# Kernel tuning notes

Hardware: AMD Instinct MI355X
Metric: run time of the kernel (lower is better)

## Reference

```python
import jax, jax.numpy as jnp
import numpy as np

VIS_DIM = 768
LBL_DIM = 128
HID = 256
VIS_W = 0.4
LBL_W = 0.6
TEMP = 1.0
EPS = 1e-12  # torch F.normalize default eps


def setup_inputs() -> dict:
    key = jax.random.key(0)
    ks = jax.random.split(key, 8)
    B, N = 32, 4096
    visual_feats = jax.random.normal(ks[0], (B, N, VIS_DIM), dtype=jnp.float32)
    label_context = jax.random.normal(ks[1], (B, LBL_DIM), dtype=jnp.float32)
    visual_mask = jnp.ones((B, N), dtype=bool)
    # scorer MLP params (stored [in, out] for x @ W)
    W1 = jax.random.normal(ks[2], (VIS_DIM, HID), dtype=jnp.float32) / np.sqrt(VIS_DIM)
    b1 = jnp.zeros((HID,), dtype=jnp.float32)
    W2 = jax.random.normal(ks[3], (HID, 1), dtype=jnp.float32) / np.sqrt(HID)
    b2 = jnp.zeros((1,), dtype=jnp.float32)
    # label -> visual projection
    Wp = jax.random.normal(ks[4], (LBL_DIM, VIS_DIM), dtype=jnp.float32) / np.sqrt(LBL_DIM)
    bp = jnp.zeros((VIS_DIM,), dtype=jnp.float32)
    return {
        "visual_feats": visual_feats,
        "label_context": label_context,
        "W1": W1, "b1": b1, "W2": W2, "b2": b2, "Wp": Wp, "bp": bp,
        "visual_mask": visual_mask,
        "k": 192,
    }


def _l2norm(x):
    n = jnp.linalg.norm(x, axis=-1, keepdims=True)
    return x / jnp.maximum(n, EPS)


def reference(visual_feats, label_context, W1, b1, W2, b2, Wp, bp, visual_mask, k):
    B, N, D = visual_feats.shape
    # scoring MLP: [B,N,D] -> [B,N]
    h = jnp.maximum(jnp.einsum('bnd,dh->bnh', visual_feats, W1) + b1, 0.0)
    visual_scores = (jnp.einsum('bnh,ho->bno', h, W2) + b2)[..., 0]
    # label projection [B,D] then cosine similarity against each patch
    label_proj = label_context @ Wp + bp              # [B, D]
    vis_n = _l2norm(visual_feats)                     # [B, N, D]
    lbl_n = _l2norm(label_proj)[:, None, :]           # [B, 1, D]
    label_scores = jnp.sum(vis_n * lbl_n, axis=-1)    # [B, N]
    combined = (VIS_W * visual_scores + LBL_W * label_scores) / TEMP
    combined = jnp.where(visual_mask, combined, -jnp.inf)
    k = min(int(k), N)
    topk_scores, topk_indices = jax.lax.top_k(combined, k)   # [B, k]
    selected_feats = jnp.take_along_axis(visual_feats, topk_indices[..., None], axis=1)
    return selected_feats, topk_indices
```

## Files before the change

kernel.cpp:

```cpp
#include <hip/hip_runtime.h>
#include <hip/hip_bf16.h>

#define B_   32
#define N_   4096
#define D_   768
#define HID_ 256

#define SX 64.0f
#define SW 1024.0f
#define INV_S (1.0f / 65536.0f)

typedef unsigned long long ull;
typedef _Float16 half8 __attribute__((ext_vector_type(8)));
typedef float f32x16 __attribute__((ext_vector_type(16)));

__global__ __launch_bounds__(256) void wsplit_kernel(
    const float* __restrict__ W1, _Float16* __restrict__ whi,
    _Float16* __restrict__ wlo) {
  int c = blockIdx.x;
  int h = threadIdx.x;
  half8 vh, vl;
#pragma unroll
  for (int j = 0; j < 8; ++j) {
    float w = W1[(size_t)(c * 8 + j) * 256 + h] * SW;
    _Float16 hi = (_Float16)w;
    vh[j] = hi;
    vl[j] = (_Float16)(w - (float)hi);
  }
  *(half8*)&whi[((size_t)c * 256 + h) * 8] = vh;
  *(half8*)&wlo[((size_t)c * 256 + h) * 8] = vl;
}

__global__ __launch_bounds__(256) void proj_norm_kernel(
    const float* __restrict__ lc, const float* __restrict__ Wp,
    const float* __restrict__ bp, float* __restrict__ lbl_n) {
  int b = blockIdx.x;
  int t = threadIdx.x;
  __shared__ float s_lc[128];
  __shared__ float s_out[768];
  __shared__ float s_red[4];

  if (t < 128) s_lc[t] = lc[b * 128 + t];
  __syncthreads();

  float sumsq = 0.f;
  for (int d = t; d < D_; d += 256) {
    float acc = bp[d];
    for (int k = 0; k < 128; ++k) acc += s_lc[k] * Wp[k * D_ + d];
    s_out[d] = acc;
    sumsq += acc * acc;
  }
  for (int off = 32; off >= 1; off >>= 1) sumsq += __shfl_xor(sumsq, off);
  if ((t & 63) == 0) s_red[t >> 6] = sumsq;
  __syncthreads();
  float tot = s_red[0] + s_red[1] + s_red[2] + s_red[3];
  float inv = 1.f / fmaxf(sqrtf(tot), 1e-12f);
  for (int d = t; d < D_; d += 256) lbl_n[b * D_ + d] = s_out[d] * inv;
}

__global__ __launch_bounds__(256, 2) void score2_kernel(
    const float* __restrict__ X, const _Float16* __restrict__ Whi,
    const _Float16* __restrict__ Wlo, const float* __restrict__ b1,
    const float* __restrict__ W2, const float* __restrict__ b2,
    const float* __restrict__ lbl_n, float* __restrict__ scores) {
  __shared__ __align__(16) _Float16 sW[2][2][4][256][8];
  __shared__ float sLbl[768];
  __shared__ float sB1[256];
  __shared__ float sW2[256];

  const int t = threadIdx.x;
  const int w = t >> 6;
  const int l = t & 63;
  const int l5 = l >> 5;
  const int ln = l & 31;
  const int pb = blockIdx.x * 128;
  const int batch = pb >> 12;
  const int patch = pb + w * 32 + ln;
  const float* xrow = X + (size_t)patch * D_;

  for (int i = t; i < D_; i += 256) sLbl[i] = lbl_n[batch * D_ + i];
  sB1[t] = b1[t];
  sW2[t] = W2[t];

  f32x16 acc[8];
#pragma unroll
  for (int mt = 0; mt < 8; ++mt)
#pragma unroll
    for (int r = 0; r < 16; ++r) acc[mt][r] = 0.f;

  const float4* gWh = (const float4*)Whi;
  const float4* gWl = (const float4*)Wlo;

  float4 wh0 = gWh[0 * 256 + t], wh1 = gWh[1 * 256 + t],
         wh2 = gWh[2 * 256 + t], wh3 = gWh[3 * 256 + t];
  float4 wl0 = gWl[0 * 256 + t], wl1 = gWl[1 * 256 + t],
         wl2 = gWl[2 * 256 + t], wl3 = gWl[3 * 256 + t];
  float4 cx0 = *(const float4*)(xrow + l5 * 8);
  float4 cx1 = *(const float4*)(xrow + l5 * 8 + 4);
  float4 cx2 = *(const float4*)(xrow + 16 + l5 * 8);
  float4 cx3 = *(const float4*)(xrow + 16 + l5 * 8 + 4);
  {
    float4* dh = (float4*)&sW[0][0][0][0][0];
    float4* dl = (float4*)&sW[0][1][0][0][0];
    dh[0 * 256 + t] = wh0; dh[1 * 256 + t] = wh1;
    dh[2 * 256 + t] = wh2; dh[3 * 256 + t] = wh3;
    dl[0 * 256 + t] = wl0; dl[1 * 256 + t] = wl1;
    dl[2 * 256 + t] = wl2; dl[3 * 256 + t] = wl3;
  }
  __syncthreads();

  float sq = 0.f, dt = 0.f;

  for (int s = 0; s < 24; ++s) {
    const int cur = s & 1;
    float4 nx0, nx1, nx2, nx3;
    if (s < 23) {
      const int sn = s + 1;
      wh0 = gWh[(size_t)sn * 1024 + 0 * 256 + t];
      wh1 = gWh[(size_t)sn * 1024 + 1 * 256 + t];
      wh2 = gWh[(size_t)sn * 1024 + 2 * 256 + t];
      wh3 = gWh[(size_t)sn * 1024 + 3 * 256 + t];
      wl0 = gWl[(size_t)sn * 1024 + 0 * 256 + t];
      wl1 = gWl[(size_t)sn * 1024 + 1 * 256 + t];
      wl2 = gWl[(size_t)sn * 1024 + 2 * 256 + t];
      wl3 = gWl[(size_t)sn * 1024 + 3 * 256 + t];
      nx0 = *(const float4*)(xrow + sn * 32 + l5 * 8);
      nx1 = *(const float4*)(xrow + sn * 32 + l5 * 8 + 4);
      nx2 = *(const float4*)(xrow + sn * 32 + 16 + l5 * 8);
      nx3 = *(const float4*)(xrow + sn * 32 + 16 + l5 * 8 + 4);
    }

#pragma unroll
    for (int ks = 0; ks < 2; ++ks) {
      float xv[8], lv[8];
      if (ks == 0) {
        xv[0] = cx0.x; xv[1] = cx0.y; xv[2] = cx0.z; xv[3] = cx0.w;
        xv[4] = cx1.x; xv[5] = cx1.y; xv[6] = cx1.z; xv[7] = cx1.w;
      } else {
        xv[0] = cx2.x; xv[1] = cx2.y; xv[2] = cx2.z; xv[3] = cx2.w;
        xv[4] = cx3.x; xv[5] = cx3.y; xv[6] = cx3.z; xv[7] = cx3.w;
      }
      const float4 lv0 = *(const float4*)&sLbl[s * 32 + ks * 16 + l5 * 8];
      const float4 lv1 = *(const float4*)&sLbl[s * 32 + ks * 16 + l5 * 8 + 4];
      lv[0] = lv0.x; lv[1] = lv0.y; lv[2] = lv0.z; lv[3] = lv0.w;
      lv[4] = lv1.x; lv[5] = lv1.y; lv[6] = lv1.z; lv[7] = lv1.w;

      half8 bh, bl;
#pragma unroll
      for (int j = 0; j < 8; ++j) {
        sq += xv[j] * xv[j];
        dt += xv[j] * lv[j];
        float xs = xv[j] * SX;
        _Float16 hi = (_Float16)xs;
        bh[j] = hi;
        bl[j] = (_Float16)(xs - (float)hi);
      }

      const int c = ks * 2 + l5;
#pragma unroll
      for (int mt = 0; mt < 8; ++mt) {
        half8 ah = *(const half8*)&sW[cur][0][c][mt * 32 + ln][0];
        half8 al = *(const half8*)&sW[cur][1][c][mt * 32 + ln][0];
        acc[mt] = __builtin_amdgcn_mfma_f32_32x32x16_f16(ah, bh, acc[mt], 0, 0, 0);
        acc[mt] = __builtin_amdgcn_mfma_f32_32x32x16_f16(ah, bl, acc[mt], 0, 0, 0);
        acc[mt] = __builtin_amdgcn_mfma_f32_32x32x16_f16(al, bh, acc[mt], 0, 0, 0);
      }
    }

    if (s < 23) {
      const int nb = cur ^ 1;
      float4* dh = (float4*)&sW[nb][0][0][0][0];
      float4* dl = (float4*)&sW[nb][1][0][0][0];
      dh[0 * 256 + t] = wh0; dh[1 * 256 + t] = wh1;
      dh[2 * 256 + t] = wh2; dh[3 * 256 + t] = wh3;
      dl[0 * 256 + t] = wl0; dl[1 * 256 + t] = wl1;
      dl[2 * 256 + t] = wl2; dl[3 * 256 + t] = wl3;
      cx0 = nx0; cx1 = nx1; cx2 = nx2; cx3 = nx3;
    }
    __syncthreads();
  }

  float vs = 0.f;
#pragma unroll
  for (int mt = 0; mt < 8; ++mt) {
#pragma unroll
    for (int rq = 0; rq < 4; ++rq) {
      const int hb = mt * 32 + rq * 8 + l5 * 4;
      const float4 b1v = *(const float4*)&sB1[hb];
      const float4 w2v = *(const float4*)&sW2[hb];
      float hv[4];
      hv[0] = acc[mt][rq * 4 + 0] * INV_S + b1v.x;
      hv[1] = acc[mt][rq * 4 + 1] * INV_S + b1v.y;
      hv[2] = acc[mt][rq * 4 + 2] * INV_S + b1v.z;
      hv[3] = acc[mt][rq * 4 + 3] * INV_S + b1v.w;
      vs += fmaxf(hv[0], 0.f) * w2v.x;
      vs += fmaxf(hv[1], 0.f) * w2v.y;
      vs += fmaxf(hv[2], 0.f) * w2v.z;
      vs += fmaxf(hv[3], 0.f) * w2v.w;
    }
  }
  vs += __shfl_xor(vs, 32);
  sq += __shfl_xor(sq, 32);
  dt += __shfl_xor(dt, 32);
  if (l < 32) {
    float lsc = dt / fmaxf(sqrtf(sq), 1e-12f);
    scores[patch] = 0.4f * (vs + b2[0]) + 0.6f * lsc;
  }
}

__global__ __launch_bounds__(256) void topk2_kernel(
    const float* __restrict__ scores, int* __restrict__ out_idx, int K) {
  int b = blockIdx.x;
  int t = threadIdx.x;
  __shared__ ull swm[4];

  ull keys[16];
#pragma unroll
  for (int j = 0; j < 16; ++j) {
    int i = (j << 8) + t;
    float s = scores[(b << 12) + i];
    unsigned u = __float_as_uint(s);
    u = (u & 0x80000000u) ? ~u : (u | 0x80000000u);
    keys[j] = ((ull)u << 32) | (unsigned)(4095 - i);
  }
  ull cur = 0;
#pragma unroll
  for (int j = 0; j < 16; ++j) cur = keys[j] > cur ? keys[j] : cur;

  for (int sel = 0; sel < K; ++sel) {
    ull wb = cur;
#pragma unroll
    for (int off = 1; off < 64; off <<= 1) {
      ull o = __shfl_xor(wb, off);
      wb = o > wb ? o : wb;
    }
    if ((t & 63) == 0) swm[t >> 6] = wb;
    __syncthreads();
    ull m0 = swm[0] > swm[1] ? swm[0] : swm[1];
    ull m1 = swm[2] > swm[3] ? swm[2] : swm[3];
    ull best = m0 > m1 ? m0 : m1;
    if (t == 0) out_idx[b * K + sel] = 4095 - (int)(unsigned)(best & 0xFFFFFFFFull);
    if (cur == best) {
      cur = 0;
#pragma unroll
      for (int j = 0; j < 16; ++j)
        cur = (keys[j] < best && keys[j] > cur) ? keys[j] : cur;
    }
    __syncthreads();
  }
}

__global__ __launch_bounds__(192) void gather_kernel(
    const float* __restrict__ feats, const int* __restrict__ idx,
    float* __restrict__ out_feats, float* __restrict__ out_idx_f, int K) {
  int i = blockIdx.x;
  int b = blockIdx.y;
  int id = idx[b * K + i];
  const float4* src = (const float4*)&feats[((size_t)b * N_ + id) * D_];
  float4* dst = (float4*)&out_feats[((size_t)b * K + i) * D_];
  dst[threadIdx.x] = src[threadIdx.x];
  if (threadIdx.x == 0) out_idx_f[b * K + i] = (float)id;
}

extern "C" void kernel_launch(void* const* d_in, const int* in_sizes, int n_in,
                              void* d_out, int out_size, void* d_ws, size_t ws_size,
                              hipStream_t stream) {
  const float* feats = (const float*)d_in[0];
  const float* lc    = (const float*)d_in[1];
  const float* W1    = (const float*)d_in[2];
  const float* b1    = (const float*)d_in[3];
  const float* W2    = (const float*)d_in[4];
  const float* b2    = (const float*)d_in[5];
  const float* Wp    = (const float*)d_in[6];
  const float* bp    = (const float*)d_in[7];
  int K = out_size / (B_ * (D_ + 1));

  float* ws_f   = (float*)d_ws;
  float* lbl_n  = ws_f;
  float* scoresv = ws_f + B_ * D_;
  int*   topidx = (int*)(ws_f + B_ * D_ + B_ * N_);
  size_t off = (size_t)B_ * D_ + (size_t)B_ * N_ + B_ * 256;
  off = (off + 3) & ~(size_t)3;
  _Float16* whi = (_Float16*)(ws_f + off);
  _Float16* wlo = whi + (size_t)96 * 256 * 8;

  float* out_f     = (float*)d_out;
  float* out_idx_f = out_f + (size_t)B_ * K * D_;

  wsplit_kernel<<<96, 256, 0, stream>>>(W1, whi, wlo);
  proj_norm_kernel<<<B_, 256, 0, stream>>>(lc, Wp, bp, lbl_n);
  score2_kernel<<<(B_ * N_) / 128, 256, 0, stream>>>(feats, whi, wlo, b1, W2, b2,
                                                     lbl_n, scoresv);
  topk2_kernel<<<B_, 256, 0, stream>>>(scoresv, topidx, K);
  gather_kernel<<<dim3(K, B_), 192, 0, stream>>>(feats, topidx, out_f, out_idx_f, K);
}
```

Baseline: 349.4 us.

## Split score kernel tile across hidden halves with shared-memory staged X

```diff
diff --git a/kernel.cpp b/kernel.cpp
--- a/kernel.cpp
+++ b/kernel.cpp
@@ -12,6 +12,7 @@
 
 typedef unsigned long long ull;
 typedef _Float16 half8 __attribute__((ext_vector_type(8)));
+typedef _Float16 half4 __attribute__((ext_vector_type(4)));
 typedef float f32x16 __attribute__((ext_vector_type(16)));
 
 __global__ __launch_bounds__(256) void wsplit_kernel(
@@ -58,153 +59,149 @@
   for (int d = t; d < D_; d += 256) lbl_n[b * D_ + d] = s_out[d] * inv;
 }
 
-__global__ __launch_bounds__(256, 2) void score2_kernel(
+__global__ __launch_bounds__(256, 3) void score3_kernel(
     const float* __restrict__ X, const _Float16* __restrict__ Whi,
     const _Float16* __restrict__ Wlo, const float* __restrict__ b1,
     const float* __restrict__ W2, const float* __restrict__ b2,
     const float* __restrict__ lbl_n, float* __restrict__ scores) {
-  __shared__ __align__(16) _Float16 sW[2][2][4][256][8];
-  __shared__ float sLbl[768];
-  __shared__ float sB1[256];
-  __shared__ float sW2[256];
-
-  const int t = threadIdx.x;
-  const int w = t >> 6;
-  const int l = t & 63;
+  __shared__ __align__(16) _Float16 sW[2][2][2][256][8];
+  __shared__ __align__(16) _Float16 sB[2][2][2][64][8];
+  __shared__ __align__(16) float sLbl[768];
+  __shared__ float sB1[256], sW2[256];
+  __shared__ float sVs[2][64];
+  __shared__ float sLsc[64];
+
+  const int t  = threadIdx.x;
+  const int w  = t >> 6;
+  const int l  = t & 63;
   const int l5 = l >> 5;
   const int ln = l & 31;
-  const int pb = blockIdx.x * 128;
+  const int pg = w & 1;
+  const int hh = w >> 1;
+  const int pb = blockIdx.x * 64;
   const int batch = pb >> 12;
-  const int patch = pb + w * 32 + ln;
-  const float* xrow = X + (size_t)patch * D_;
 
   for (int i = t; i < D_; i += 256) sLbl[i] = lbl_n[batch * D_ + i];
   sB1[t] = b1[t];
   sW2[t] = W2[t];
 
-  f32x16 acc[8];
-#pragma unroll
-  for (int mt = 0; mt < 8; ++mt)
+  const int srow = t >> 2;
+  const int sk   = t & 3;
+  const float* xrow = X + (size_t)(pb + srow) * D_;
+
+  f32x16 acc[4];
+#pragma unroll
+  for (int mt = 0; mt < 4; ++mt)
 #pragma unroll
     for (int r = 0; r < 16; ++r) acc[mt][r] = 0.f;
 
   const float4* gWh = (const float4*)Whi;
   const float4* gWl = (const float4*)Wlo;
 
-  float4 wh0 = gWh[0 * 256 + t], wh1 = gWh[1 * 256 + t],
-         wh2 = gWh[2 * 256 + t], wh3 = gWh[3 * 256 + t];
-  float4 wl0 = gWl[0 * 256 + t], wl1 = gWl[1 * 256 + t],
-         wl2 = gWl[2 * 256 + t], wl3 = gWl[3 * 256 + t];
-  float4 cx0 = *(const float4*)(xrow + l5 * 8);
-  float4 cx1 = *(const float4*)(xrow + l5 * 8 + 4);
-  float4 cx2 = *(const float4*)(xrow + 16 + l5 * 8);
-  float4 cx3 = *(const float4*)(xrow + 16 + l5 * 8 + 4);
+  float sq = 0.f, dt = 0.f;
+
+  float4 wh0 = gWh[t],        wh1 = gWh[256 + t];
+  float4 wl0 = gWl[t],        wl1 = gWl[256 + t];
+  float4 xr  = *(const float4*)&xrow[sk * 4];
+
+  __syncthreads();
+
   {
+    float4 lv = *(const float4*)&sLbl[sk * 4];
+    half4 h_, l_;
+#pragma unroll
+    for (int j = 0; j < 4; ++j) {
+      float xv = (&xr.x)[j];
+      sq += xv * xv;
+      dt += xv * (&lv.x)[j];
+      float xs = xv * SX;
+      _Float16 hi = (_Float16)xs;
+      h_[j] = hi;
+      l_[j] = (_Float16)(xs - (float)hi);
+    }
+    *(half4*)&sB[0][0][sk >> 1][srow][(sk & 1) * 4] = h_;
+    *(half4*)&sB[0][1][sk >> 1][srow][(sk & 1) * 4] = l_;
     float4* dh = (float4*)&sW[0][0][0][0][0];
     float4* dl = (float4*)&sW[0][1][0][0][0];
-    dh[0 * 256 + t] = wh0; dh[1 * 256 + t] = wh1;
-    dh[2 * 256 + t] = wh2; dh[3 * 256 + t] = wh3;
-    dl[0 * 256 + t] = wl0; dl[1 * 256 + t] = wl1;
-    dl[2 * 256 + t] = wl2; dl[3 * 256 + t] = wl3;
-  }
-  __syncthreads();
-
-  float sq = 0.f, dt = 0.f;
-
-  for (int s = 0; s < 24; ++s) {
+    dh[t] = wh0; dh[256 + t] = wh1;
+    dl[t] = wl0; dl[256 + t] = wl1;
+  }
+  __syncthreads();
+
+  for (int s = 0; s < 48; ++s) {
     const int cur = s & 1;
-    float4 nx0, nx1, nx2, nx3;
-    if (s < 23) {
+    if (s < 47) {
       const int sn = s + 1;
-      wh0 = gWh[(size_t)sn * 1024 + 0 * 256 + t];
-      wh1 = gWh[(size_t)sn * 1024 + 1 * 256 + t];
-      wh2 = gWh[(size_t)sn * 1024 + 2 * 256 + t];
-      wh3 = gWh[(size_t)sn * 1024 + 3 * 256 + t];
-      wl0 = gWl[(size_t)sn * 1024 + 0 * 256 + t];
-      wl1 = gWl[(size_t)sn * 1024 + 1 * 256 + t];
-      wl2 = gWl[(size_t)sn * 1024 + 2 * 256 + t];
-      wl3 = gWl[(size_t)sn * 1024 + 3 * 256 + t];
-      nx0 = *(const float4*)(xrow + sn * 32 + l5 * 8);
-      nx1 = *(const float4*)(xrow + sn * 32 + l5 * 8 + 4);
-      nx2 = *(const float4*)(xrow + sn * 32 + 16 + l5 * 8);
-      nx3 = *(const float4*)(xrow + sn * 32 + 16 + l5 * 8 + 4);
-    }
-
-#pragma unroll
-    for (int ks = 0; ks < 2; ++ks) {
-      float xv[8], lv[8];
-      if (ks == 0) {
-        xv[0] = cx0.x; xv[1] = cx0.y; xv[2] = cx0.z; xv[3] = cx0.w;
-        xv[4] = cx1.x; xv[5] = cx1.y; xv[6] = cx1.z; xv[7] = cx1.w;
-      } else {
-        xv[0] = cx2.x; xv[1] = cx2.y; xv[2] = cx2.z; xv[3] = cx2.w;
-        xv[4] = cx3.x; xv[5] = cx3.y; xv[6] = cx3.z; xv[7] = cx3.w;
+      wh0 = gWh[sn * 512 + t];       wh1 = gWh[sn * 512 + 256 + t];
+      wl0 = gWl[sn * 512 + t];       wl1 = gWl[sn * 512 + 256 + t];
+      xr  = *(const float4*)&xrow[sn * 16 + sk * 4];
+    }
+
+    half8 bh = *(const half8*)&sB[cur][0][l5][pg * 32 + ln][0];
+    half8 bl = *(const half8*)&sB[cur][1][l5][pg * 32 + ln][0];
+#pragma unroll
+    for (int mt = 0; mt < 4; ++mt) {
+      half8 ah = *(const half8*)&sW[cur][0][l5][hh * 128 + mt * 32 + ln][0];
+      half8 al = *(const half8*)&sW[cur][1][l5][hh * 128 + mt * 32 + ln][0];
+      acc[mt] = __builtin_amdgcn_mfma_f32_32x32x16_f16(ah, bh, acc[mt], 0, 0, 0);
+      acc[mt] = __builtin_amdgcn_mfma_f32_32x32x16_f16(ah, bl, acc[mt], 0, 0, 0);
+      acc[mt] = __builtin_amdgcn_mfma_f32_32x32x16_f16(al, bh, acc[mt], 0, 0, 0);
+    }
+
+    if (s < 47) {
+      const int nb = cur ^ 1;
+      float4 lv = *(const float4*)&sLbl[(s + 1) * 16 + sk * 4];
+      half4 h_, l_;
+#pragma unroll
+      for (int j = 0; j < 4; ++j) {
+        float xv = (&xr.x)[j];
+        sq += xv * xv;
+        dt += xv * (&lv.x)[j];
+        float xs = xv * SX;
+        _Float16 hi = (_Float16)xs;
+        h_[j] = hi;
+        l_[j] = (_Float16)(xs - (float)hi);
       }
-      const float4 lv0 = *(const float4*)&sLbl[s * 32 + ks * 16 + l5 * 8];
-      const float4 lv1 = *(const float4*)&sLbl[s * 32 + ks * 16 + l5 * 8 + 4];
-      lv[0] = lv0.x; lv[1] = lv0.y; lv[2] = lv0.z; lv[3] = lv0.w;
-      lv[4] = lv1.x; lv[5] = lv1.y; lv[6] = lv1.z; lv[7] = lv1.w;
-
-      half8 bh, bl;
-#pragma unroll
-      for (int j = 0; j < 8; ++j) {
-        sq += xv[j] * xv[j];
-        dt += xv[j] * lv[j];
-        float xs = xv[j] * SX;
-        _Float16 hi = (_Float16)xs;
-        bh[j] = hi;
-        bl[j] = (_Float16)(xs - (float)hi);
-      }
-
-      const int c = ks * 2 + l5;
-#pragma unroll
-      for (int mt = 0; mt < 8; ++mt) {
-        half8 ah = *(const half8*)&sW[cur][0][c][mt * 32 + ln][0];
-        half8 al = *(const half8*)&sW[cur][1][c][mt * 32 + ln][0];
-        acc[mt] = __builtin_amdgcn_mfma_f32_32x32x16_f16(ah, bh, acc[mt], 0, 0, 0);
-        acc[mt] = __builtin_amdgcn_mfma_f32_32x32x16_f16(ah, bl, acc[mt], 0, 0, 0);
-        acc[mt] = __builtin_amdgcn_mfma_f32_32x32x16_f16(al, bh, acc[mt], 0, 0, 0);
-      }
-    }
-
-    if (s < 23) {
-      const int nb = cur ^ 1;
+      *(half4*)&sB[nb][0][sk >> 1][srow][(sk & 1) * 4] = h_;
+      *(half4*)&sB[nb][1][sk >> 1][srow][(sk & 1) * 4] = l_;
       float4* dh = (float4*)&sW[nb][0][0][0][0];
       float4* dl = (float4*)&sW[nb][1][0][0][0];
-      dh[0 * 256 + t] = wh0; dh[1 * 256 + t] = wh1;
-      dh[2 * 256 + t] = wh2; dh[3 * 256 + t] = wh3;
-      dl[0 * 256 + t] = wl0; dl[1 * 256 + t] = wl1;
-      dl[2 * 256 + t] = wl2; dl[3 * 256 + t] = wl3;
-      cx0 = nx0; cx1 = nx1; cx2 = nx2; cx3 = nx3;
+      dh[t] = wh0; dh[256 + t] = wh1;
+      dl[t] = wl0; dl[256 + t] = wl1;
     }
     __syncthreads();
   }
 
+  sq += __shfl_xor(sq, 1); dt += __shfl_xor(dt, 1);
+  sq += __shfl_xor(sq, 2); dt += __shfl_xor(dt, 2);
+  if ((l & 3) == 0) sLsc[srow] = dt / fmaxf(sqrtf(sq), 1e-12f);
+
   float vs = 0.f;
 #pragma unroll
-  for (int mt = 0; mt < 8; ++mt) {
+  for (int mt = 0; mt < 4; ++mt) {
 #pragma unroll
     for (int rq = 0; rq < 4; ++rq) {
-      const int hb = mt * 32 + rq * 8 + l5 * 4;
+      const int hb = hh * 128 + mt * 32 + rq * 8 + l5 * 4;
       const float4 b1v = *(const float4*)&sB1[hb];
       const float4 w2v = *(const float4*)&sW2[hb];
-      float hv[4];
-      hv[0] = acc[mt][rq * 4 + 0] * INV_S + b1v.x;
-      hv[1] = acc[mt][rq * 4 + 1] * INV_S + b1v.y;
-      hv[2] = acc[mt][rq * 4 + 2] * INV_S + b1v.z;
-      hv[3] = acc[mt][rq * 4 + 3] * INV_S + b1v.w;
-      vs += fmaxf(hv[0], 0.f) * w2v.x;
-      vs += fmaxf(hv[1], 0.f) * w2v.y;
-      vs += fmaxf(hv[2], 0.f) * w2v.z;
-      vs += fmaxf(hv[3], 0.f) * w2v.w;
+      float hv0 = acc[mt][rq * 4 + 0] * INV_S + b1v.x;
+      float hv1 = acc[mt][rq * 4 + 1] * INV_S + b1v.y;
+      float hv2 = acc[mt][rq * 4 + 2] * INV_S + b1v.z;
+      float hv3 = acc[mt][rq * 4 + 3] * INV_S + b1v.w;
+      vs += fmaxf(hv0, 0.f) * w2v.x;
+      vs += fmaxf(hv1, 0.f) * w2v.y;
+      vs += fmaxf(hv2, 0.f) * w2v.z;
+      vs += fmaxf(hv3, 0.f) * w2v.w;
     }
   }
   vs += __shfl_xor(vs, 32);
-  sq += __shfl_xor(sq, 32);
-  dt += __shfl_xor(dt, 32);
-  if (l < 32) {
-    float lsc = dt / fmaxf(sqrtf(sq), 1e-12f);
-    scores[patch] = 0.4f * (vs + b2[0]) + 0.6f * lsc;
+  if (l < 32) sVs[hh][pg * 32 + l] = vs;
+  __syncthreads();
+
+  if (w < 2 && l < 32) {
+    int p = w * 32 + l;
+    float vst = sVs[0][p] + sVs[1][p] + b2[0];
+    scores[pb + p] = 0.4f * vst + 0.6f * sLsc[p];
   }
 }
 
@@ -275,10 +272,10 @@
   const float* bp    = (const float*)d_in[7];
   int K = out_size / (B_ * (D_ + 1));
 
-  float* ws_f   = (float*)d_ws;
-  float* lbl_n  = ws_f;
+  float* ws_f    = (float*)d_ws;
+  float* lbl_n   = ws_f;
   float* scoresv = ws_f + B_ * D_;
-  int*   topidx = (int*)(ws_f + B_ * D_ + B_ * N_);
+  int*   topidx  = (int*)(ws_f + B_ * D_ + B_ * N_);
   size_t off = (size_t)B_ * D_ + (size_t)B_ * N_ + B_ * 256;
   off = (off + 3) & ~(size_t)3;
   _Float16* whi = (_Float16*)(ws_f + off);
@@ -289,8 +286,8 @@
 
   wsplit_kernel<<<96, 256, 0, stream>>>(W1, whi, wlo);
   proj_norm_kernel<<<B_, 256, 0, stream>>>(lc, Wp, bp, lbl_n);
-  score2_kernel<<<(B_ * N_) / 128, 256, 0, stream>>>(feats, whi, wlo, b1, W2, b2,
-                                                     lbl_n, scoresv);
+  score3_kernel<<<(B_ * N_) / 64, 256, 0, stream>>>(feats, whi, wlo, b1, W2, b2,
+                                                    lbl_n, scoresv);
   topk2_kernel<<<B_, 256, 0, stream>>>(scoresv, topidx, K);
   gather_kernel<<<dim3(K, B_), 192, 0, stream>>>(feats, topidx, out_f, out_idx_f, K);
 }
```

Measured after the change: 399.2 us. 1.14x slower.
